# Kernel optimization log

Measured on AMD Instinct MI355X. Metric: run time of the kernel, lower is better.

## Reference

```python
import jax, jax.numpy as jnp
import numpy as np

K_NEIGHBORS = 20


def setup_inputs() -> dict:
    key = jax.random.key(0)
    ks = jax.random.split(key, 13)
    B, C, N = 8, 3, 4096
    s = lambda k_, shape, fan: jax.random.normal(k_, shape, jnp.float32) * (1.0 / np.sqrt(fan))
    return {
        "x": jax.random.normal(ks[0], (B, C, N), jnp.float32),
        "W1": s(ks[1], (64, 6), 6),      "b1": jnp.zeros((64,), jnp.float32),
        "W2": s(ks[2], (128, 64), 64),   "b2": jnp.zeros((128,), jnp.float32),
        "Wi": s(ks[3], (1024, 128), 128),"bi": jnp.zeros((1024,), jnp.float32),
        "Wg1": s(ks[4], (512, 1024), 1024), "bg1": jnp.zeros((512,), jnp.float32),
        "Wg2": s(ks[5], (256, 512), 512),   "bg2": jnp.zeros((256,), jnp.float32),
        "Wl": s(ks[6], (9, 256), 256),      "bl": jnp.zeros((9,), jnp.float32),
    }


def _tnet(x, W1, b1, W2, b2, Wi, bi, Wg1, bg1, Wg2, bg2, Wl, bl):
    B, C, N = x.shape
    # pairwise squared distance: ||xi||^2 - 2 xi.xj + ||xj||^2  -> (B, N, N)
    inner = jnp.einsum("bcn,bcm->bnm", x, x)
    sq = jnp.sum(x * x, axis=1)  # (B, N)
    dist = sq[:, :, None] - 2.0 * inner + sq[:, None, :]
    # k nearest neighbours (smallest distance)
    _, knn = jax.lax.top_k(-dist, K_NEIGHBORS)  # (B, N, k)
    # gather neighbour features directly (no (B,C,N,N) tile)
    central = x[:, :, :, None]                                   # (B, C, N, 1)
    neigh = jnp.take_along_axis(x[:, :, None, :], knn[:, None, :, :], axis=-1)  # (B, C, N, k)
    edge = jnp.concatenate(
        [jnp.broadcast_to(central, neigh.shape), neigh - central], axis=1
    )  # (B, 2C, N, k)
    # local 1x1 conv2d blocks (conv + relu)
    h = jax.nn.relu(jnp.einsum("oc,bcnk->bonk", W1, edge) + b1[None, :, None, None])
    h = jax.nn.relu(jnp.einsum("oc,bcnk->bonk", W2, h) + b2[None, :, None, None])
    h = jnp.max(h, axis=-1)  # max over k -> (B, 128, N)
    # inter 1x1 conv1d block
    h = jax.nn.relu(jnp.einsum("oc,bcn->bon", Wi, h) + bi[None, :, None])
    g = jnp.max(h, axis=-1)  # global max over nodes -> (B, 1024)
    # global MLP
    g = jax.nn.relu(g @ Wg1.T + bg1)
    g = jax.nn.relu(g @ Wg2.T + bg2)
    out = g @ Wl.T + bl  # (B, 9)
    out = out.reshape(B, 3, 3) + jnp.eye(3, dtype=out.dtype)
    return out


def reference(x, W1, b1, W2, b2, Wi, bi, Wg1, bg1, Wg2, bg2, Wl, bl):
    return _tnet(x, W1, b1, W2, b2, Wi, bi, Wg1, bg1, Wg2, bg2, Wl, bl)
```

## Files before the change

kernel.cpp:

```cpp
#include <hip/hip_runtime.h>
#include <stdint.h>

typedef unsigned long long u64;
typedef unsigned short ushort_t;
#define NPTS 4096
#define KNN 20

using bf16x8 = __attribute__((ext_vector_type(8))) short;
using f32x4  = __attribute__((ext_vector_type(4))) float;
using f32x2  = __attribute__((ext_vector_type(2))) float;

__device__ __forceinline__ unsigned orderbits(float f) {
  unsigned u = __float_as_uint(f);
  return ((int)u < 0) ? ~u : (u | 0x80000000u);
}

__device__ __forceinline__ ushort_t f2bf(float f) {
  unsigned u = __float_as_uint(f);
  u += 0x7fffu + ((u >> 16) & 1u);
  return (ushort_t)(u >> 16);
}

__device__ __forceinline__ u64 shflxor64(u64 v, int m) {
  unsigned lo = __shfl_xor((unsigned)(v & 0xffffffffull), m, 64);
  unsigned hi = __shfl_xor((unsigned)(v >> 32), m, 64);
  return (((u64)hi) << 32) | lo;
}

__device__ __forceinline__ float dist_exact(float4 q, float4 a) {
  float inner = __fadd_rn(__fadd_rn(__fmul_rn(q.x, a.x), __fmul_rn(q.y, a.y)),
                          __fmul_rn(q.z, a.z));
  return __fadd_rn(__fsub_rn(q.w, __fmul_rn(2.0f, inner)), a.w);
}

__device__ __forceinline__ f32x2 dist2(f32x2 qx, f32x2 qy, f32x2 qz, f32x2 qw,
                                       float4 a) {
#pragma clang fp contract(off)
  f32x2 ax = {a.x, a.x}, ay = {a.y, a.y}, az = {a.z, a.z}, aw = {a.w, a.w};
  f32x2 t0 = qx * ax;
  f32x2 t1 = qy * ay;
  f32x2 t2 = qz * az;
  f32x2 inner = (t0 + t1) + t2;
  f32x2 two = {2.0f, 2.0f};
  return (qw - two * inner) + aw;
}

__device__ __forceinline__ unsigned bucket_of(float d) {
  unsigned bits = __float_as_uint(fmaxf(d, 0.f));
  int t = (int)(bits >> 19) - 1840;
  return (unsigned)min(max(t, 0), 511);
}

__global__ __launch_bounds__(256) void setup_kernel(
    const float* __restrict__ x, const float* __restrict__ Wi,
    const float* __restrict__ W2, float4* __restrict__ xT4,
    ushort_t* __restrict__ wiB, ushort_t* __restrict__ w2B,
    unsigned* __restrict__ g) {
  int i = blockIdx.x * 256 + threadIdx.x;
  wiB[i] = f2bf(Wi[i]);
  if (i < 32768) {
    int b = i >> 12, m = i & 4095;
    const float* xb = x + (size_t)b * 3 * NPTS;
    float a0 = xb[m], a1 = xb[NPTS + m], a2 = xb[2 * NPTS + m];
    float sq = __fadd_rn(__fadd_rn(__fmul_rn(a0, a0), __fmul_rn(a1, a1)),
                         __fmul_rn(a2, a2));
    xT4[i] = make_float4(a0, a1, a2, sq);
  }
  if (i < 8192) { w2B[i] = f2bf(W2[i]); g[i] = 0u; }
}

#define NB 512
#define PPB 4
#define CCAP 128
__global__ __launch_bounds__(256) void knn_kernel(const float4* __restrict__ xT4,
                                                  int* __restrict__ knn_out) {
  __shared__ unsigned hist[PPB * NB];
  __shared__ u64 cand[PPB * CCAP];
  __shared__ unsigned sB[PPB], sCnt[PPB], sCand[PPB];

  const int tid = threadIdx.x;
  const int bid = blockIdx.x;
  const int b = bid >> 10;
  const int n0 = (bid & 1023) * PPB;
  const float4* xb4 = xT4 + (size_t)b * NPTS;

  float4 q[PPB];
#pragma unroll
  for (int p = 0; p < PPB; ++p) q[p] = xb4[n0 + p];
  const f32x2 qx01 = {q[0].x, q[1].x}, qy01 = {q[0].y, q[1].y},
              qz01 = {q[0].z, q[1].z}, qw01 = {q[0].w, q[1].w};
  const f32x2 qx23 = {q[2].x, q[3].x}, qy23 = {q[2].y, q[3].y},
              qz23 = {q[2].z, q[3].z}, qw23 = {q[2].w, q[3].w};

  for (int i = tid; i < PPB * NB; i += 256) hist[i] = 0;
  if (tid < PPB) { sCnt[tid] = 0; sCand[tid] = 0; }
  __syncthreads();

  unsigned kL[16], kH[16];
#pragma unroll 4
  for (int it = 0; it < 16; ++it) {
    const int m = it * 256 + tid;
    float4 a = xb4[m];
    f32x2 d01 = dist2(qx01, qy01, qz01, qw01, a);
    f32x2 d23 = dist2(qx23, qy23, qz23, qw23, a);
    unsigned bk0 = bucket_of(d01[0]);
    unsigned bk1 = bucket_of(d01[1]);
    unsigned bk2 = bucket_of(d23[0]);
    unsigned bk3 = bucket_of(d23[1]);
    atomicAdd(&hist[0 * NB + bk0], 1u);
    atomicAdd(&hist[1 * NB + bk1], 1u);
    atomicAdd(&hist[2 * NB + bk2], 1u);
    atomicAdd(&hist[3 * NB + bk3], 1u);
    kL[it] = bk0 | (bk1 << 16);
    kH[it] = bk2 | (bk3 << 16);
  }
  __syncthreads();

  const int lane = tid & 63, wv = tid >> 6;
  {
    unsigned h[8]; unsigned local = 0;
    const int hb = wv * NB + lane * 8;
#pragma unroll
    for (int j = 0; j < 8; ++j) { h[j] = hist[hb + j]; local += h[j]; }
    unsigned incl = local;
    for (int off = 1; off < 64; off <<= 1) {
      unsigned v = __shfl_up(incl, off, 64);
      if (lane >= off) incl += v;
    }
    unsigned excl = incl - local;
    if (excl < KNN && incl >= KNN) {
      unsigned cum = excl;
#pragma unroll
      for (int j = 0; j < 8; ++j) {
        if (cum + h[j] >= KNN) { sB[wv] = lane * 8 + j; break; }
        cum += h[j];
      }
    }
  }
  __syncthreads();

  const unsigned B0 = sB[0], B1 = sB[1], B2 = sB[2], B3 = sB[3];
  for (int it = 0; it < 16; ++it) {
    const int m = it * 256 + tid;
    unsigned ks[PPB];
    ks[0] = kL[it] & 0xffffu; ks[1] = kL[it] >> 16;
    ks[2] = kH[it] & 0xffffu; ks[3] = kH[it] >> 16;
    unsigned Bs[PPB] = {B0, B1, B2, B3};
#pragma unroll
    for (int p = 0; p < PPB; ++p) {
      if (ks[p] < Bs[p]) {
        unsigned s = atomicAdd(&sCnt[p], 1u);
        knn_out[((size_t)((b << 12) + n0 + p)) * KNN + s] = m;
      } else if (ks[p] == Bs[p]) {
        float d = dist_exact(q[p], xb4[m]);
        unsigned s = atomicAdd(&sCand[p], 1u);
        if (s < CCAP) cand[p * CCAP + s] = (((u64)orderbits(d)) << 32) | (unsigned)m;
      }
    }
  }
  __syncthreads();

  {
    const int nsel = (int)sCnt[wv];
    const int ncand = min((int)sCand[wv], CCAP);
    const int ntake = KNN - nsel;
    const size_t base = ((size_t)((b << 12) + n0 + wv)) * KNN;
    volatile u64* vc = &cand[wv * CCAP];
    for (int t = 0; t < ntake; ++t) {
      u64 mk = ~0ull;
      for (int i = lane; i < ncand; i += 64) { u64 v = vc[i]; if (v < mk) mk = v; }
      for (int off = 32; off; off >>= 1) { u64 o = shflxor64(mk, off); if (o < mk) mk = o; }
      if (lane == 0) knn_out[base + nsel + t] = (int)(unsigned)(mk & 0xffffffffull);
      for (int i = lane; i < ncand; i += 64) { if (vc[i] == mk) vc[i] = ~0ull; }
    }
  }
}

__global__ __launch_bounds__(256, 4) void edge_fused(
    const float4* __restrict__ xT4, const int* __restrict__ knn,
    const float* __restrict__ W1, const float* __restrict__ b1,
    const ushort_t* __restrict__ w2B, const float* __restrict__ b2,
    ushort_t* __restrict__ hT) {
  __shared__ __align__(16) ushort_t h1S[4 * 32 * 64];
  __shared__ __align__(16) ushort_t w2S[128 * 64];
  const int tid = threadIdx.x;
  const int lane = tid & 63, wv = tid >> 6;
  const int ln = lane & 15, quad = lane >> 4;

  if (tid < 128) {
    const int p = tid >> 5, s5 = tid & 31;
    const int idx = blockIdx.x * 4 + p;
    const int b = idx >> 12, n = idx & 4095;
    const float4* xb4 = xT4 + ((size_t)b << 12);
    const float4 c4 = xb4[n];
    const int c0 = 2 * s5;
    float w1a[6], w1b[6];
#pragma unroll
    for (int j = 0; j < 6; ++j) {
      w1a[j] = W1[c0 * 6 + j];
      w1b[j] = W1[(c0 + 1) * 6 + j];
    }
    const float b1a = b1[c0], b1b = b1[c0 + 1];
    const int kbase = idx * KNN;
    unsigned* h1d = (unsigned*)h1S;
#pragma unroll 4
    for (int k = 0; k < KNN; ++k) {
      int nb = knn[kbase + k];
      float4 a4 = xb4[nb];
      float e3 = a4.x - c4.x, e4 = a4.y - c4.y, e5 = a4.z - c4.z;
      float za = b1a, zb = b1b;
      za = fmaf(w1a[0], c4.x, za); zb = fmaf(w1b[0], c4.x, zb);
      za = fmaf(w1a[1], c4.y, za); zb = fmaf(w1b[1], c4.y, zb);
      za = fmaf(w1a[2], c4.z, za); zb = fmaf(w1b[2], c4.z, zb);
      za = fmaf(w1a[3], e3, za);   zb = fmaf(w1b[3], e3, zb);
      za = fmaf(w1a[4], e4, za);   zb = fmaf(w1b[4], e4, zb);
      za = fmaf(w1a[5], e5, za);   zb = fmaf(w1b[5], e5, zb);
      unsigned pk = (unsigned)f2bf(fmaxf(za, 0.f)) |
                    ((unsigned)f2bf(fmaxf(zb, 0.f)) << 16);
      int row = p * 32 + k;
      int dw = row * 32 + (((s5 >> 2) ^ (row & 7)) << 2) + (s5 & 3);
      h1d[dw] = pk;
    }
  } else {
    const int t = tid - 128;
    const int4* wg = (const int4*)w2B;
#pragma unroll
    for (int j = 0; j < 8; ++j) {
      int qq = j * 128 + t;
      int row = qq >> 3, c = qq & 7;
      ((int4*)w2S)[row * 8 + (c ^ (row & 7))] = wg[qq];
    }
  }
  float b2r[8];
#pragma unroll
  for (int n = 0; n < 8; ++n) b2r[n] = b2[n * 16 + ln];
  __syncthreads();

  bf16x8 Bf[8][2];
#pragma unroll
  for (int n = 0; n < 8; ++n)
#pragma unroll
    for (int s = 0; s < 2; ++s) {
      int row = n * 16 + ln;
      Bf[n][s] = *(const bf16x8*)&w2S[row * 64 + (((s * 4 + quad) ^ (ln & 7)) << 3)];
    }

  const int ps = wv;
  const int sw = ln & 7;
  float vmax[8];
  {
    const int row = ps * 32 + ln;
    bf16x8 A0 = *(const bf16x8*)&h1S[row * 64 + (((0 + quad) ^ sw) << 3)];
    bf16x8 A1 = *(const bf16x8*)&h1S[row * 64 + (((4 + quad) ^ sw) << 3)];
    f32x4 acc;
#pragma unroll
    for (int n = 0; n < 8; ++n) {
      acc = (f32x4){0.f, 0.f, 0.f, 0.f};
      acc = __builtin_amdgcn_mfma_f32_16x16x32_bf16(A0, Bf[n][0], acc, 0, 0, 0);
      acc = __builtin_amdgcn_mfma_f32_16x16x32_bf16(A1, Bf[n][1], acc, 0, 0, 0);
      vmax[n] = fmaxf(fmaxf(acc[0], acc[1]), fmaxf(acc[2], acc[3]));
    }
  }
  {
    const int row = ps * 32 + 16 + ln;
    bf16x8 A0 = *(const bf16x8*)&h1S[row * 64 + (((0 + quad) ^ sw) << 3)];
    bf16x8 A1 = *(const bf16x8*)&h1S[row * 64 + (((4 + quad) ^ sw) << 3)];
    f32x4 acc;
#pragma unroll
    for (int n = 0; n < 8; ++n) {
      acc = (f32x4){0.f, 0.f, 0.f, 0.f};
      acc = __builtin_amdgcn_mfma_f32_16x16x32_bf16(A0, Bf[n][0], acc, 0, 0, 0);
      acc = __builtin_amdgcn_mfma_f32_16x16x32_bf16(A1, Bf[n][1], acc, 0, 0, 0);
      float v1 = (quad == 0)
                     ? fmaxf(fmaxf(acc[0], acc[1]), fmaxf(acc[2], acc[3]))
                     : -INFINITY;
      vmax[n] = fmaxf(vmax[n], v1);
    }
  }
  const int gidx = blockIdx.x * 4 + ps;
#pragma unroll
  for (int n = 0; n < 8; ++n) {
    float v = vmax[n];
    v = fmaxf(v, __shfl_xor(v, 16, 64));
    v = fmaxf(v, __shfl_xor(v, 32, 64));
    if (quad == 0) {
      hT[(size_t)gidx * 128 + n * 16 + ln] = f2bf(fmaxf(v + b2r[n], 0.f));
    }
  }
}

#define LDP 136
__global__ __launch_bounds__(256, 2) void inception_mfma(
    const ushort_t* __restrict__ hT, const ushort_t* __restrict__ wiB,
    const float* __restrict__ bi, unsigned* __restrict__ g) {
  __shared__ __align__(16) ushort_t hS[128 * LDP];
  __shared__ __align__(16) ushort_t wS[128 * LDP];
  const int tid = threadIdx.x;
  const int b = blockIdx.z;
  const int m0 = blockIdx.x * 128;
  const int n0 = blockIdx.y * 128;

  const ushort_t* hg = hT + ((size_t)b * NPTS + m0) * 128;
  const ushort_t* wg = wiB + (size_t)n0 * 128;
#pragma unroll
  for (int i = 0; i < 8; ++i) {
    int chunk = i * 256 + tid;
    int row = chunk >> 4, c = chunk & 15;
    *(int4*)&hS[row * LDP + c * 8] = *(const int4*)&hg[row * 128 + c * 8];
    *(int4*)&wS[row * LDP + c * 8] = *(const int4*)&wg[row * 128 + c * 8];
  }
  __syncthreads();

  const int lane = tid & 63, wid = tid >> 6;
  const int ln = lane & 15, quad = lane >> 4;
  const int mw = (wid >> 1) * 64, nw = (wid & 1) * 64;

  f32x4 acc[4][4];
#pragma unroll
  for (int mi = 0; mi < 4; ++mi)
#pragma unroll
    for (int ni = 0; ni < 4; ++ni) acc[mi][ni] = (f32x4){0.f, 0.f, 0.f, 0.f};

#pragma unroll
  for (int kk = 0; kk < 4; ++kk) {
    bf16x8 af[4], bfr[4];
    const int ko = kk * 32 + quad * 8;
#pragma unroll
    for (int mi = 0; mi < 4; ++mi)
      af[mi] = *(const bf16x8*)&hS[(mw + mi * 16 + ln) * LDP + ko];
#pragma unroll
    for (int ni = 0; ni < 4; ++ni)
      bfr[ni] = *(const bf16x8*)&wS[(nw + ni * 16 + ln) * LDP + ko];
#pragma unroll
    for (int mi = 0; mi < 4; ++mi)
#pragma unroll
      for (int ni = 0; ni < 4; ++ni)
        acc[mi][ni] = __builtin_amdgcn_mfma_f32_16x16x32_bf16(
            af[mi], bfr[ni], acc[mi][ni], 0, 0, 0);
  }

#pragma unroll
  for (int ni = 0; ni < 4; ++ni) {
    float v = acc[0][ni][0];
#pragma unroll
    for (int mi = 0; mi < 4; ++mi)
#pragma unroll
      for (int r = 0; r < 4; ++r) v = fmaxf(v, acc[mi][ni][r]);
    v = fmaxf(v, __shfl_xor(v, 16, 64));
    v = fmaxf(v, __shfl_xor(v, 32, 64));
    if (quad == 0) {
      int o = n0 + nw + ni * 16 + ln;
      float val = fmaxf(v + bi[o], 0.f);
      atomicMax(&g[b * 1024 + o], __float_as_uint(val));
    }
  }
}

__global__ __launch_bounds__(256) void head1_kernel(
    const unsigned* __restrict__ g, const float* __restrict__ Wg1,
    const float* __restrict__ bg1, float* __restrict__ g1) {
  const int b = blockIdx.x >> 3, slice = blockIdx.x & 7;
  const int tid = threadIdx.x;
  const int ol = tid >> 2, part = tid & 3;
  const int o = slice * 64 + ol;
  const float4* w = (const float4*)(Wg1 + (size_t)o * 1024 + part * 256);
  const float4* gv = (const float4*)((const float*)(g + b * 1024) + part * 256);
  float a0 = 0.f, a1 = 0.f, a2 = 0.f, a3 = 0.f;
#pragma unroll
  for (int j = 0; j < 64; j += 4) {
    float4 w0 = w[j], w1 = w[j+1], w2 = w[j+2], w3 = w[j+3];
    float4 v0 = gv[j], v1 = gv[j+1], v2 = gv[j+2], v3 = gv[j+3];
    a0 = fmaf(w0.x, v0.x, a0); a0 = fmaf(w0.y, v0.y, a0);
    a0 = fmaf(w0.z, v0.z, a0); a0 = fmaf(w0.w, v0.w, a0);
    a1 = fmaf(w1.x, v1.x, a1); a1 = fmaf(w1.y, v1.y, a1);
    a1 = fmaf(w1.z, v1.z, a1); a1 = fmaf(w1.w, v1.w, a1);
    a2 = fmaf(w2.x, v2.x, a2); a2 = fmaf(w2.y, v2.y, a2);
    a2 = fmaf(w2.z, v2.z, a2); a2 = fmaf(w2.w, v2.w, a2);
    a3 = fmaf(w3.x, v3.x, a3); a3 = fmaf(w3.y, v3.y, a3);
    a3 = fmaf(w3.z, v3.z, a3); a3 = fmaf(w3.w, v3.w, a3);
  }
  float s = (a0 + a1) + (a2 + a3);
  s += __shfl_xor(s, 1, 64);
  s += __shfl_xor(s, 2, 64);
  if (part == 0) g1[b * 512 + o] = fmaxf(s + bg1[o], 0.f);
}

__global__ __launch_bounds__(256) void head2_kernel(
    const float* __restrict__ g1, const float* __restrict__ Wg2,
    const float* __restrict__ bg2, const float* __restrict__ Wl,
    const float* __restrict__ bl, float* __restrict__ out) {
  __shared__ __align__(16) float g1l[512];
  __shared__ __align__(16) float g2l[256];
  const int tid = threadIdx.x;
  const int b = blockIdx.x;
  g1l[tid] = g1[b * 512 + tid];
  g1l[tid + 256] = g1[b * 512 + 256 + tid];
  __syncthreads();
  {
    const float4* w = (const float4*)(Wg2 + (size_t)tid * 512);
    const float4* gv = (const float4*)g1l;
    float a0 = bg2[tid], a1 = 0.f;
    for (int j = 0; j < 128; j += 2) {
      float4 w0 = w[j], w1 = w[j+1];
      float4 v0 = gv[j], v1 = gv[j+1];
      a0 = fmaf(w0.x, v0.x, a0); a0 = fmaf(w0.y, v0.y, a0);
      a0 = fmaf(w0.z, v0.z, a0); a0 = fmaf(w0.w, v0.w, a0);
      a1 = fmaf(w1.x, v1.x, a1); a1 = fmaf(w1.y, v1.y, a1);
      a1 = fmaf(w1.z, v1.z, a1); a1 = fmaf(w1.w, v1.w, a1);
    }
    g2l[tid] = fmaxf(a0 + a1, 0.f);
  }
  __syncthreads();
  if (tid < 9) {
    float acc = bl[tid];
    for (int c = 0; c < 256; ++c) acc = fmaf(Wl[tid * 256 + c], g2l[c], acc);
    if (tid == 0 || tid == 4 || tid == 8) acc += 1.0f;
    out[b * 9 + tid] = acc;
  }
}

extern "C" void kernel_launch(void* const* d_in, const int* in_sizes, int n_in,
                              void* d_out, int out_size, void* d_ws, size_t ws_size,
                              hipStream_t stream) {
  const float* x   = (const float*)d_in[0];
  const float* W1  = (const float*)d_in[1];
  const float* b1  = (const float*)d_in[2];
  const float* W2  = (const float*)d_in[3];
  const float* b2  = (const float*)d_in[4];
  const float* Wi  = (const float*)d_in[5];
  const float* bi  = (const float*)d_in[6];
  const float* Wg1 = (const float*)d_in[7];
  const float* bg1 = (const float*)d_in[8];
  const float* Wg2 = (const float*)d_in[9];
  const float* bg2 = (const float*)d_in[10];
  const float* Wl  = (const float*)d_in[11];
  const float* bl  = (const float*)d_in[12];

  int*       knn = (int*)d_ws;
  ushort_t*  hT  = (ushort_t*)((char*)d_ws + (3u << 20));
  ushort_t*  wiB = (ushort_t*)((char*)d_ws + (12u << 20));
  ushort_t*  w2B = (ushort_t*)((char*)d_ws + (12u << 20) + (512u << 10));
  float4*    xT4 = (float4*)((char*)d_ws + (13u << 20));
  unsigned*  g   = (unsigned*)((char*)d_ws + (14u << 20));
  float*     g1  = (float*)((char*)d_ws + (14u << 20) + (64u << 10));

  setup_kernel<<<512, 256, 0, stream>>>(x, Wi, W2, xT4, wiB, w2B, g);
  knn_kernel<<<8 * NPTS / PPB, 256, 0, stream>>>(xT4, knn);
  edge_fused<<<8 * NPTS / 4, 256, 0, stream>>>(xT4, knn, W1, b1, w2B, b2, hT);
  inception_mfma<<<dim3(32, 8, 8), 256, 0, stream>>>(hT, wiB, bi, g);
  head1_kernel<<<64, 256, 0, stream>>>(g, Wg1, bg1, g1);
  head2_kernel<<<8, 256, 0, stream>>>(g1, Wg2, bg2, Wl, bl, (float*)d_out);
}
```

Measured before the change: 267.3 us.

## Rebalance edge conv threads and loop inception over all output tiles per block

```diff
diff --git a/kernel.cpp b/kernel.cpp
--- a/kernel.cpp
+++ b/kernel.cpp
@@ -187,48 +187,47 @@
   const int lane = tid & 63, wv = tid >> 6;
   const int ln = lane & 15, quad = lane >> 4;
 
-  if (tid < 128) {
-    const int p = tid >> 5, s5 = tid & 31;
+  {
+    const int4* wg = (const int4*)w2B;
+#pragma unroll
+    for (int j = 0; j < 4; ++j) {
+      int qq = j * 256 + tid;
+      int row = qq >> 3, c = qq & 7;
+      ((int4*)w2S)[row * 8 + (c ^ (row & 7))] = wg[qq];
+    }
+  }
+
+  {
+    const int p = wv, ch = lane;
     const int idx = blockIdx.x * 4 + p;
     const int b = idx >> 12, n = idx & 4095;
     const float4* xb4 = xT4 + ((size_t)b << 12);
     const float4 c4 = xb4[n];
-    const int c0 = 2 * s5;
-    float w1a[6], w1b[6];
-#pragma unroll
-    for (int j = 0; j < 6; ++j) {
-      w1a[j] = W1[c0 * 6 + j];
-      w1b[j] = W1[(c0 + 1) * 6 + j];
-    }
-    const float b1a = b1[c0], b1b = b1[c0 + 1];
-    const int kbase = idx * KNN;
-    unsigned* h1d = (unsigned*)h1S;
+    float w1r[6];
+#pragma unroll
+    for (int j = 0; j < 6; ++j) w1r[j] = W1[ch * 6 + j];
+    const float b1r = b1[ch];
+    const int4* kb = (const int4*)&knn[idx * KNN];
+    int4 i0 = kb[0], i1 = kb[1], i2 = kb[2], i3 = kb[3], i4 = kb[4];
+    int nb[20] = {i0.x, i0.y, i0.z, i0.w, i1.x, i1.y, i1.z, i1.w,
+                  i2.x, i2.y, i2.z, i2.w, i3.x, i3.y, i3.z, i3.w,
+                  i4.x, i4.y, i4.z, i4.w};
+    const int swz = ((ch >> 3) ^ 7) * 0;
+    (void)swz;
 #pragma unroll 4
     for (int k = 0; k < KNN; ++k) {
-      int nb = knn[kbase + k];
-      float4 a4 = xb4[nb];
+      float4 a4 = xb4[nb[k]];
       float e3 = a4.x - c4.x, e4 = a4.y - c4.y, e5 = a4.z - c4.z;
-      float za = b1a, zb = b1b;
-      za = fmaf(w1a[0], c4.x, za); zb = fmaf(w1b[0], c4.x, zb);
-      za = fmaf(w1a[1], c4.y, za); zb = fmaf(w1b[1], c4.y, zb);
-      za = fmaf(w1a[2], c4.z, za); zb = fmaf(w1b[2], c4.z, zb);
-      za = fmaf(w1a[3], e3, za);   zb = fmaf(w1b[3], e3, zb);
-      za = fmaf(w1a[4], e4, za);   zb = fmaf(w1b[4], e4, zb);
-      za = fmaf(w1a[5], e5, za);   zb = fmaf(w1b[5], e5, zb);
-      unsigned pk = (unsigned)f2bf(fmaxf(za, 0.f)) |
-                    ((unsigned)f2bf(fmaxf(zb, 0.f)) << 16);
+      float z = b1r;
+      z = fmaf(w1r[0], c4.x, z);
+      z = fmaf(w1r[1], c4.y, z);
+      z = fmaf(w1r[2], c4.z, z);
+      z = fmaf(w1r[3], e3, z);
+      z = fmaf(w1r[4], e4, z);
+      z = fmaf(w1r[5], e5, z);
       int row = p * 32 + k;
-      int dw = row * 32 + (((s5 >> 2) ^ (row & 7)) << 2) + (s5 & 3);
-      h1d[dw] = pk;
-    }
-  } else {
-    const int t = tid - 128;
-    const int4* wg = (const int4*)w2B;
-#pragma unroll
-    for (int j = 0; j < 8; ++j) {
-      int qq = j * 128 + t;
-      int row = qq >> 3, c = qq & 7;
-      ((int4*)w2S)[row * 8 + (c ^ (row & 7))] = wg[qq];
+      int u16i = row * 64 + (((ch >> 3) ^ (row & 7)) << 3) + (ch & 7);
+      h1S[u16i] = f2bf(fmaxf(z, 0.f));
     }
   }
   float b2r[8];
@@ -294,64 +293,67 @@
     const ushort_t* __restrict__ hT, const ushort_t* __restrict__ wiB,
     const float* __restrict__ bi, unsigned* __restrict__ g) {
   __shared__ __align__(16) ushort_t hS[128 * LDP];
-  __shared__ __align__(16) ushort_t wS[128 * LDP];
   const int tid = threadIdx.x;
-  const int b = blockIdx.z;
+  const int b = blockIdx.y;
   const int m0 = blockIdx.x * 128;
-  const int n0 = blockIdx.y * 128;
 
   const ushort_t* hg = hT + ((size_t)b * NPTS + m0) * 128;
-  const ushort_t* wg = wiB + (size_t)n0 * 128;
 #pragma unroll
   for (int i = 0; i < 8; ++i) {
     int chunk = i * 256 + tid;
     int row = chunk >> 4, c = chunk & 15;
     *(int4*)&hS[row * LDP + c * 8] = *(const int4*)&hg[row * 128 + c * 8];
-    *(int4*)&wS[row * LDP + c * 8] = *(const int4*)&wg[row * 128 + c * 8];
   }
   __syncthreads();
 
   const int lane = tid & 63, wid = tid >> 6;
   const int ln = lane & 15, quad = lane >> 4;
-  const int mw = (wid >> 1) * 64, nw = (wid & 1) * 64;
-
-  f32x4 acc[4][4];
-#pragma unroll
-  for (int mi = 0; mi < 4; ++mi)
-#pragma unroll
-    for (int ni = 0; ni < 4; ++ni) acc[mi][ni] = (f32x4){0.f, 0.f, 0.f, 0.f};
-
-#pragma unroll
-  for (int kk = 0; kk < 4; ++kk) {
-    bf16x8 af[4], bfr[4];
-    const int ko = kk * 32 + quad * 8;
+  const int mw = (wid >> 1) * 64, nwo = (wid & 1) * 64;
+
+  bf16x8 af[4][4];
+#pragma unroll
+  for (int kk = 0; kk < 4; ++kk)
 #pragma unroll
     for (int mi = 0; mi < 4; ++mi)
-      af[mi] = *(const bf16x8*)&hS[(mw + mi * 16 + ln) * LDP + ko];
+      af[kk][mi] = *(const bf16x8*)&hS[(mw + mi * 16 + ln) * LDP + kk * 32 + quad * 8];
+
+  for (int n0t = 0; n0t < 8; ++n0t) {
+    const int n0 = n0t * 128;
+    bf16x8 bfr[4][4];
 #pragma unroll
     for (int ni = 0; ni < 4; ++ni)
-      bfr[ni] = *(const bf16x8*)&wS[(nw + ni * 16 + ln) * LDP + ko];
+#pragma unroll
+      for (int kk = 0; kk < 4; ++kk)
+        bfr[ni][kk] = *(const bf16x8*)&wiB[(size_t)(n0 + nwo + ni * 16 + ln) * 128 +
+                                           kk * 32 + quad * 8];
+    f32x4 acc[4][4];
 #pragma unroll
     for (int mi = 0; mi < 4; ++mi)
 #pragma unroll
-      for (int ni = 0; ni < 4; ++ni)
-        acc[mi][ni] = __builtin_amdgcn_mfma_f32_16x16x32_bf16(
-            af[mi], bfr[ni], acc[mi][ni], 0, 0, 0);
-  }
-
-#pragma unroll
-  for (int ni = 0; ni < 4; ++ni) {
-    float v = acc[0][ni][0];
-#pragma unroll
-    for (int mi = 0; mi < 4; ++mi)
-#pragma unroll
-      for (int r = 0; r < 4; ++r) v = fmaxf(v, acc[mi][ni][r]);
-    v = fmaxf(v, __shfl_xor(v, 16, 64));
-    v = fmaxf(v, __shfl_xor(v, 32, 64));
-    if (quad == 0) {
-      int o = n0 + nw + ni * 16 + ln;
-      float val = fmaxf(v + bi[o], 0.f);
-      atomicMax(&g[b * 1024 + o], __float_as_uint(val));
+      for (int ni = 0; ni < 4; ++ni) acc[mi][ni] = (f32x4){0.f, 0.f, 0.f, 0.f};
+#pragma unroll
+    for (int kk = 0; kk < 4; ++kk)
+#pragma unroll
+      for (int mi = 0; mi < 4; ++mi)
+#pragma unroll
+        for (int ni = 0; ni < 4; ++ni)
+          acc[mi][ni] = __builtin_amdgcn_mfma_f32_16x16x32_bf16(
+              af[kk][mi], bfr[ni][kk], acc[mi][ni], 0, 0, 0);
+
+#pragma unroll
+    for (int ni = 0; ni < 4; ++ni) {
+      float v = acc[0][ni][0];
+#pragma unroll
+      for (int mi = 0; mi < 4; ++mi)
+#pragma unroll
+        for (int r = 0; r < 4; ++r) v = fmaxf(v, acc[mi][ni][r]);
+      v = fmaxf(v, __shfl_xor(v, 16, 64));
+      v = fmaxf(v, __shfl_xor(v, 32, 64));
+      if (quad == 0) {
+        int o = n0 + nwo + ni * 16 + ln;
+        float val = fmaxf(v + bi[o], 0.f);
+        atomicMax(&g[b * 1024 + o], __float_as_uint(val));
+      }
     }
   }
 }
@@ -447,7 +449,7 @@
   setup_kernel<<<512, 256, 0, stream>>>(x, Wi, W2, xT4, wiB, w2B, g);
   knn_kernel<<<8 * NPTS / PPB, 256, 0, stream>>>(xT4, knn);
   edge_fused<<<8 * NPTS / 4, 256, 0, stream>>>(xT4, knn, W1, b1, w2B, b2, hT);
-  inception_mfma<<<dim3(32, 8, 8), 256, 0, stream>>>(hT, wiB, bi, g);
+  inception_mfma<<<dim3(32, 8), 256, 0, stream>>>(hT, wiB, bi, g);
   head1_kernel<<<64, 256, 0, stream>>>(g, Wg1, bg1, g1);
   head2_kernel<<<8, 256, 0, stream>>>(g1, Wg2, bg2, Wl, bl, (float*)d_out);
 }
```

Result: slower. 283.8 us (+6.2%).

## Process eight query points per KNN block with coarser 256-bucket histograms

Applied to the files above, without the earlier changes.

```diff
diff --git a/kernel.cpp b/kernel.cpp
--- a/kernel.cpp
+++ b/kernel.cpp
@@ -47,8 +47,8 @@
 
 __device__ __forceinline__ unsigned bucket_of(float d) {
   unsigned bits = __float_as_uint(fmaxf(d, 0.f));
-  int t = (int)(bits >> 19) - 1840;
-  return (unsigned)min(max(t, 0), 511);
+  int t = (int)(bits >> 20) - 920;
+  return (unsigned)min(max(t, 0), 255);
 }
 
 __global__ __launch_bounds__(256) void setup_kernel(
@@ -69,10 +69,10 @@
   if (i < 8192) { w2B[i] = f2bf(W2[i]); g[i] = 0u; }
 }
 
-#define NB 512
-#define PPB 4
+#define NB 256
+#define PPB 8
 #define CCAP 128
-__global__ __launch_bounds__(256) void knn_kernel(const float4* __restrict__ xT4,
+__global__ __launch_bounds__(512) void knn_kernel(const float4* __restrict__ xT4,
                                                   int* __restrict__ knn_out) {
   __shared__ unsigned hist[PPB * NB];
   __shared__ u64 cand[PPB * CCAP];
@@ -80,48 +80,54 @@
 
   const int tid = threadIdx.x;
   const int bid = blockIdx.x;
-  const int b = bid >> 10;
-  const int n0 = (bid & 1023) * PPB;
+  const int b = bid >> 9;
+  const int n0 = (bid & 511) * PPB;
   const float4* xb4 = xT4 + (size_t)b * NPTS;
 
-  float4 q[PPB];
-#pragma unroll
-  for (int p = 0; p < PPB; ++p) q[p] = xb4[n0 + p];
-  const f32x2 qx01 = {q[0].x, q[1].x}, qy01 = {q[0].y, q[1].y},
-              qz01 = {q[0].z, q[1].z}, qw01 = {q[0].w, q[1].w};
-  const f32x2 qx23 = {q[2].x, q[3].x}, qy23 = {q[2].y, q[3].y},
-              qz23 = {q[2].z, q[3].z}, qw23 = {q[2].w, q[3].w};
-
-  for (int i = tid; i < PPB * NB; i += 256) hist[i] = 0;
+  f32x2 qx[4], qy[4], qz[4], qw[4];
+#pragma unroll
+  for (int j = 0; j < 4; ++j) {
+    float4 qa = xb4[n0 + 2 * j], qb = xb4[n0 + 2 * j + 1];
+    qx[j] = (f32x2){qa.x, qb.x}; qy[j] = (f32x2){qa.y, qb.y};
+    qz[j] = (f32x2){qa.z, qb.z}; qw[j] = (f32x2){qa.w, qb.w};
+  }
+
+  for (int i = tid; i < PPB * NB; i += 512) hist[i] = 0;
   if (tid < PPB) { sCnt[tid] = 0; sCand[tid] = 0; }
   __syncthreads();
 
-  unsigned kL[16], kH[16];
+  unsigned kA[8], kB[8];
 #pragma unroll 4
-  for (int it = 0; it < 16; ++it) {
-    const int m = it * 256 + tid;
+  for (int it = 0; it < 8; ++it) {
+    const int m = it * 512 + tid;
     float4 a = xb4[m];
-    f32x2 d01 = dist2(qx01, qy01, qz01, qw01, a);
-    f32x2 d23 = dist2(qx23, qy23, qz23, qw23, a);
-    unsigned bk0 = bucket_of(d01[0]);
-    unsigned bk1 = bucket_of(d01[1]);
-    unsigned bk2 = bucket_of(d23[0]);
-    unsigned bk3 = bucket_of(d23[1]);
-    atomicAdd(&hist[0 * NB + bk0], 1u);
-    atomicAdd(&hist[1 * NB + bk1], 1u);
-    atomicAdd(&hist[2 * NB + bk2], 1u);
-    atomicAdd(&hist[3 * NB + bk3], 1u);
-    kL[it] = bk0 | (bk1 << 16);
-    kH[it] = bk2 | (bk3 << 16);
+    f32x2 d01 = dist2(qx[0], qy[0], qz[0], qw[0], a);
+    f32x2 d23 = dist2(qx[1], qy[1], qz[1], qw[1], a);
+    f32x2 d45 = dist2(qx[2], qy[2], qz[2], qw[2], a);
+    f32x2 d67 = dist2(qx[3], qy[3], qz[3], qw[3], a);
+    unsigned b0 = bucket_of(d01[0]), b1 = bucket_of(d01[1]);
+    unsigned b2 = bucket_of(d23[0]), b3 = bucket_of(d23[1]);
+    unsigned b4 = bucket_of(d45[0]), b5 = bucket_of(d45[1]);
+    unsigned b6 = bucket_of(d67[0]), b7 = bucket_of(d67[1]);
+    atomicAdd(&hist[0 * NB + b0], 1u);
+    atomicAdd(&hist[1 * NB + b1], 1u);
+    atomicAdd(&hist[2 * NB + b2], 1u);
+    atomicAdd(&hist[3 * NB + b3], 1u);
+    atomicAdd(&hist[4 * NB + b4], 1u);
+    atomicAdd(&hist[5 * NB + b5], 1u);
+    atomicAdd(&hist[6 * NB + b6], 1u);
+    atomicAdd(&hist[7 * NB + b7], 1u);
+    kA[it] = b0 | (b1 << 8) | (b2 << 16) | (b3 << 24);
+    kB[it] = b4 | (b5 << 8) | (b6 << 16) | (b7 << 24);
   }
   __syncthreads();
 
   const int lane = tid & 63, wv = tid >> 6;
   {
-    unsigned h[8]; unsigned local = 0;
-    const int hb = wv * NB + lane * 8;
-#pragma unroll
-    for (int j = 0; j < 8; ++j) { h[j] = hist[hb + j]; local += h[j]; }
+    unsigned h[4]; unsigned local = 0;
+    const int hb = wv * NB + lane * 4;
+#pragma unroll
+    for (int j = 0; j < 4; ++j) { h[j] = hist[hb + j]; local += h[j]; }
     unsigned incl = local;
     for (int off = 1; off < 64; off <<= 1) {
       unsigned v = __shfl_up(incl, off, 64);
@@ -131,28 +137,29 @@
     if (excl < KNN && incl >= KNN) {
       unsigned cum = excl;
 #pragma unroll
-      for (int j = 0; j < 8; ++j) {
-        if (cum + h[j] >= KNN) { sB[wv] = lane * 8 + j; break; }
+      for (int j = 0; j < 4; ++j) {
+        if (cum + h[j] >= KNN) { sB[wv] = lane * 4 + j; break; }
         cum += h[j];
       }
     }
   }
   __syncthreads();
 
-  const unsigned B0 = sB[0], B1 = sB[1], B2 = sB[2], B3 = sB[3];
-  for (int it = 0; it < 16; ++it) {
-    const int m = it * 256 + tid;
-    unsigned ks[PPB];
-    ks[0] = kL[it] & 0xffffu; ks[1] = kL[it] >> 16;
-    ks[2] = kH[it] & 0xffffu; ks[3] = kH[it] >> 16;
-    unsigned Bs[PPB] = {B0, B1, B2, B3};
+  unsigned Bs[PPB];
+#pragma unroll
+  for (int p = 0; p < PPB; ++p) Bs[p] = sB[p];
+
+  for (int it = 0; it < 8; ++it) {
+    const int m = it * 512 + tid;
+    const unsigned ka = kA[it], kb = kB[it];
 #pragma unroll
     for (int p = 0; p < PPB; ++p) {
-      if (ks[p] < Bs[p]) {
+      unsigned ks = ((p < 4 ? ka : kb) >> (8 * (p & 3))) & 255u;
+      if (ks < Bs[p]) {
         unsigned s = atomicAdd(&sCnt[p], 1u);
         knn_out[((size_t)((b << 12) + n0 + p)) * KNN + s] = m;
-      } else if (ks[p] == Bs[p]) {
-        float d = dist_exact(q[p], xb4[m]);
+      } else if (ks == Bs[p]) {
+        float d = dist_exact(xb4[n0 + p], xb4[m]);
         unsigned s = atomicAdd(&sCand[p], 1u);
         if (s < CCAP) cand[p * CCAP + s] = (((u64)orderbits(d)) << 32) | (unsigned)m;
       }
@@ -445,7 +452,7 @@
   float*     g1  = (float*)((char*)d_ws + (14u << 20) + (64u << 10));
 
   setup_kernel<<<512, 256, 0, stream>>>(x, Wi, W2, xT4, wiB, w2B, g);
-  knn_kernel<<<8 * NPTS / PPB, 256, 0, stream>>>(xT4, knn);
+  knn_kernel<<<8 * NPTS / PPB, 512, 0, stream>>>(xT4, knn);
   edge_fused<<<8 * NPTS / 4, 256, 0, stream>>>(xT4, knn, W1, b1, w2B, b2, hT);
   inception_mfma<<<dim3(32, 8, 8), 256, 0, stream>>>(hT, wiB, bi, g);
   head1_kernel<<<64, 256, 0, stream>>>(g, Wg1, bg1, g1);
```

New measurement: 283.3 us. 1.06x slower.
